# Optimization experiments

Measured on AMD Instinct MI355X. Metric: run time of the kernel, lower is better.

Reference implementation:

```python
import jax, jax.numpy as jnp
import numpy as np

# Static problem sizes (see shape_source)
B, SX, SY = 256, 256, 70          # graphs, encoder nodes/graph, decoder nodes/graph
F, EMB, H = 512, 256, 256          # f_size, emb_size, h_size
VOCAB = 256
E = 4 * B * SY                     # 71680 edges
N_SLT = 4                          # SltEdgeTypes
N_SRT = 8                          # len(SrtEdgeTypes)


def setup_inputs() -> dict:
    key = jax.random.key(0)
    ks = jax.random.split(key, 24)
    s = 0.02
    inp = {
        'x': jax.random.normal(ks[0], (B * SX, F), jnp.float32),
        'x_batch': jnp.repeat(jnp.arange(B, dtype=jnp.int64), SX),
        'tgt_y': jax.random.randint(ks[1], (B * SY,), 0, VOCAB, jnp.int64),
        'tgt_edge_index': jax.random.randint(ks[2], (2, E), 0, B * SY, jnp.int64),
        'tgt_edge_type': jax.random.randint(ks[3], (E,), 0, N_SLT, jnp.int64),
        'tgt_y_batch': jnp.repeat(jnp.arange(B, dtype=jnp.int64), SY),
        'embeds': jax.random.normal(ks[4], (VOCAB, EMB), jnp.float32) * s,
    }
    dims = [(EMB, H), (H, H), (H, EMB)]
    k = 5
    for l, (din, dout) in enumerate(dims, start=1):
        inp[f'W_in{l}'] = jax.random.normal(ks[k + 0], (din, dout), jnp.float32) * s
        inp[f'Wq{l}'] = jax.random.normal(ks[k + 1], (dout, F), jnp.float32) * s
        inp[f'Wv{l}'] = jax.random.normal(ks[k + 2], (F, dout), jnp.float32) * s
        inp[f'Ee{l}'] = jax.random.normal(ks[k + 3], (N_SLT, dout), jnp.float32) * s
        k += 4
    inp['lin_z_w'] = jax.random.normal(ks[k], (EMB, VOCAB), jnp.float32) * s
    inp['lin_z_b'] = jnp.zeros((VOCAB,), jnp.float32)
    inp['lin_g_w'] = jax.random.normal(ks[k + 1], (2 * EMB, N_SRT), jnp.float32) * s
    inp['lin_g_b'] = jnp.zeros((N_SRT,), jnp.float32)
    return inp


def gcn_dec_layer(x_b, y, src, tgt, etype, W_in, Wq, Wv, Ee):
    """Edge-type-conditioned message passing + cross-attention onto encoder x.
    x_b: [B,SX,F]; y: [Ny,din]. Returns ([Ny,dout], alpha [B,SY,SX])."""
    h = y @ W_in                                   # [Ny, dout]
    m = h[src] + Ee[etype]                         # gather + type embedding
    agg = jax.ops.segment_sum(m, tgt, num_segments=y.shape[0])
    q = (h @ Wq).reshape(B, SY, F)                 # query into encoder space
    logits = jnp.einsum('bqf,bkf->bqk', q, x_b) / jnp.sqrt(jnp.float32(F))
    alpha = jax.nn.softmax(logits, axis=-1)        # [B,SY,SX]
    ctx = jnp.einsum('bqk,bkf->bqf', alpha, x_b) @ Wv  # [B,SY,dout]
    out = jax.nn.relu(h + agg + ctx.reshape(h.shape[0], -1))
    return out, alpha


def reference(x, x_batch, tgt_y, tgt_edge_index, tgt_edge_type, tgt_y_batch,
              embeds, W_in1, Wq1, Wv1, Ee1, W_in2, Wq2, Wv2, Ee2,
              W_in3, Wq3, Wv3, Ee3, lin_z_w, lin_z_b, lin_g_w, lin_g_b):
    x_b = x.reshape(B, SX, F)
    src, tgt = tgt_edge_index[0], tgt_edge_index[1]
    y = embeds[tgt_y]                              # [Ny, EMB]
    y, a1 = gcn_dec_layer(x_b, y, src, tgt, tgt_edge_type, W_in1, Wq1, Wv1, Ee1)
    y, a2 = gcn_dec_layer(x_b, y, src, tgt, tgt_edge_type, W_in2, Wq2, Wv2, Ee2)
    y, a3 = gcn_dec_layer(x_b, y, src, tgt, tgt_edge_type, W_in3, Wq3, Wv3, Ee3)
    y_score = y @ lin_z_w + lin_z_b                # [Ny, VOCAB]
    ef = y[tgt_edge_index]                         # [2, E, EMB]
    ef = jnp.transpose(ef, (1, 0, 2)).reshape(E, 2 * EMB)
    y_edge_rel_score = ef @ lin_g_w + lin_g_b      # [E, N_SRT]
    return (y, y_score, y_edge_rel_score, a1, a2, a3)
```

## Files before the change

### kernel.cpp

```cpp
#include <hip/hip_runtime.h>
#include <cstddef>
#include <cstdint>

#define B_    256
#define SX_   256
#define SY_   70
#define F_    512
#define EMB_  256
#define NY_   (B_*SY_)
#define NE_   (4*B_*SY_)

typedef short s16x8 __attribute__((ext_vector_type(8)));
typedef float f32x4 __attribute__((ext_vector_type(4)));
typedef unsigned short us4 __attribute__((ext_vector_type(4)));
typedef unsigned short us8 __attribute__((ext_vector_type(8)));

__device__ __forceinline__ unsigned short f2bf(float f) {
    unsigned u = __builtin_bit_cast(unsigned, f);
    u += 0x7fffu + ((u >> 16) & 1u);
    return (unsigned short)(u >> 16);
}
__device__ __forceinline__ float bf2f(unsigned short b) {
    unsigned u = ((unsigned)b) << 16;
    return __builtin_bit_cast(float, u);
}

template<int EPI, int SWZ>
__global__ __launch_bounds__(256, 2)
void gemm_mfma(const unsigned short* __restrict__ A, int lda, long sAb,
               const unsigned short* __restrict__ Bt, int ldb, long sBb,
               float* __restrict__ Cf, int ldc, long sCfb,
               unsigned short* __restrict__ Cb, int ldcb, long sCbb,
               const float* __restrict__ aux1, long sAux,
               int M, int K, float scale, int nx, int ny)
{
    __shared__ unsigned short As[128 * 64];
    __shared__ unsigned short Bs[128 * 64];
    char* AsB = (char*)As;
    char* BsB = (char*)Bs;
    const int tid = threadIdx.x;
    int bxi, byi, z;
    if (SWZ) {
        const int nwg = gridDim.x;
        const int bid = blockIdx.x;
        const int wg = (bid & 7) * (nwg >> 3) + (bid >> 3);
        bxi = wg % nx;
        byi = (wg / nx) % ny;
        z   = wg / (nx * ny);
    } else {
        bxi = blockIdx.x; byi = blockIdx.y; z = blockIdx.z;
    }
    A  += (size_t)z * sAb;
    Bt += (size_t)z * sBb;
    const char* auxp = (const char*)aux1 + (size_t)z * sAux;
    const int bm = byi * 128, bn = bxi * 128;
    const int lane = tid & 63;
    const int w = tid >> 6, wr = w >> 1, wc = w & 1;
    const int l15 = lane & 15, lq = lane >> 4;

    f32x4 acc[4][4];
    const f32x4 z4 = {0.f, 0.f, 0.f, 0.f};
#pragma unroll
    for (int m = 0; m < 4; ++m)
#pragma unroll
        for (int n = 0; n < 4; ++n) acc[m][n] = z4;

    for (int k0 = 0; k0 < K; k0 += 64) {
#pragma unroll
        for (int i = 0; i < 4; ++i) {
            const int row = i * 32 + (tid >> 3);
            const int k8  = (tid & 7) ^ (row & 7);
            int ra = bm + row; ra = (ra < M) ? ra : (M - 1);
            const unsigned short* g = A + (size_t)ra * lda + k0 + k8 * 8;
            __builtin_amdgcn_global_load_lds(
                (const __attribute__((address_space(1))) unsigned int*)g,
                (__attribute__((address_space(3))) unsigned int*)(AsB + i * 4096 + tid * 16),
                16, 0, 0);
        }
#pragma unroll
        for (int i = 0; i < 4; ++i) {
            const int row = i * 32 + (tid >> 3);
            const int k8  = (tid & 7) ^ (row & 7);
            const unsigned short* g = Bt + (size_t)(bn + row) * ldb + k0 + k8 * 8;
            __builtin_amdgcn_global_load_lds(
                (const __attribute__((address_space(1))) unsigned int*)g,
                (__attribute__((address_space(3))) unsigned int*)(BsB + i * 4096 + tid * 16),
                16, 0, 0);
        }
        __syncthreads();
#pragma unroll
        for (int kk = 0; kk < 2; ++kk) {
            s16x8 af[4], bf[4];
#pragma unroll
            for (int m = 0; m < 4; ++m) {
                const int row = wr * 64 + m * 16 + l15;
                const int slot = (kk * 4 + lq) ^ (row & 7);
                af[m] = *(const s16x8*)(AsB + row * 128 + slot * 16);
            }
#pragma unroll
            for (int n = 0; n < 4; ++n) {
                const int col = wc * 64 + n * 16 + l15;
                const int slot = (kk * 4 + lq) ^ (col & 7);
                bf[n] = *(const s16x8*)(BsB + col * 128 + slot * 16);
            }
#pragma unroll
            for (int m = 0; m < 4; ++m)
#pragma unroll
                for (int n = 0; n < 4; ++n)
                    acc[m][n] = __builtin_amdgcn_mfma_f32_16x16x32_bf16(
                        af[m], bf[n], acc[m][n], 0, 0, 0);
        }
        __syncthreads();
    }

    float* cf = Cf ? Cf + (size_t)z * sCfb : nullptr;
    unsigned short* cb = Cb ? Cb + (size_t)z * sCbb : nullptr;
#pragma unroll
    for (int m = 0; m < 4; ++m) {
#pragma unroll
        for (int n = 0; n < 4; ++n) {
            const int col = bn + wc * 64 + n * 16 + l15;
            f32x4 v = acc[m][n];
#pragma unroll
            for (int r = 0; r < 4; ++r) {
                const int gr = bm + wr * 64 + m * 16 + lq * 4 + r;
                if (gr >= M) continue;
                float o = v[r] * scale;
                if (EPI == 4) o += ((const float*)auxp)[col];
                if (EPI == 7) {
                    if (col < 256) cb[(size_t)gr * ldcb + col] = f2bf(o);
                    else ((unsigned short*)cf)[(size_t)gr * 512 + (col - 256)] = f2bf(o);
                } else {
                    if (cf) cf[(size_t)gr * ldc + col] = o;
                    if (cb) cb[(size_t)gr * ldcb + col] = f2bf(o);
                }
            }
        }
    }
}

template<int LAST>
__global__ __launch_bounds__(512, 1)
void attn_pv(const unsigned short* __restrict__ Q,
             const unsigned short* __restrict__ X,
             const unsigned short* __restrict__ XV,
             long sXVb,
             const unsigned short* __restrict__ aggb,
             const unsigned short* __restrict__ lzT,
             const float* __restrict__ lzb,
             const float* __restrict__ gw,
             float* __restrict__ Y12g,
             float* __restrict__ Aout,
             unsigned short* __restrict__ Yb,
             float* __restrict__ Yf,
             float* __restrict__ Score,
             float scale)
{
    __shared__ unsigned short As[128 * 64];
    __shared__ unsigned short Bs[256 * 64];
    __shared__ unsigned short Al[128 * 256];
    __shared__ float red[4][2][64];
    char* AsB = (char*)As;
    char* BsB = (char*)Bs;
    char* AlB = (char*)Al;
    const int tid = threadIdx.x;
    const int z = blockIdx.x;
    const unsigned short* Qb  = Q + (size_t)z * SY_ * F_;
    const unsigned short* Xb  = X + (size_t)z * SX_ * F_;
    const unsigned short* xvb = XV + (size_t)z * sXVb;
    const int lane = tid & 63;
    const int w = tid >> 6, wr = w >> 2, wc = w & 3;
    const int l15 = lane & 15, lq = lane >> 4;

    f32x4 acc[4][4];
    const f32x4 z4 = {0.f, 0.f, 0.f, 0.f};
#pragma unroll
    for (int m = 0; m < 4; ++m)
#pragma unroll
        for (int n = 0; n < 4; ++n) acc[m][n] = z4;

    for (int k0 = 0; k0 < F_; k0 += 64) {
#pragma unroll
        for (int i = 0; i < 2; ++i) {
            const int row = i * 64 + (tid >> 3);
            const int k8  = (tid & 7) ^ (row & 7);
            const int ra = (row < SY_) ? row : (SY_ - 1);
            const unsigned short* g = Qb + (size_t)ra * F_ + k0 + k8 * 8;
            __builtin_amdgcn_global_load_lds(
                (const __attribute__((address_space(1))) unsigned int*)g,
                (__attribute__((address_space(3))) unsigned int*)(AsB + i * 8192 + tid * 16),
                16, 0, 0);
        }
#pragma unroll
        for (int i = 0; i < 4; ++i) {
            const int row = i * 64 + (tid >> 3);
            const int k8  = (tid & 7) ^ (row & 7);
            const unsigned short* g = Xb + (size_t)row * F_ + k0 + k8 * 8;
            __builtin_amdgcn_global_load_lds(
                (const __attribute__((address_space(1))) unsigned int*)g,
                (__attribute__((address_space(3))) unsigned int*)(BsB + i * 8192 + tid * 16),
                16, 0, 0);
        }
        __syncthreads();
#pragma unroll
        for (int kk = 0; kk < 2; ++kk) {
            s16x8 af[4], bf[4];
#pragma unroll
            for (int m = 0; m < 4; ++m) {
                const int row = wr * 64 + m * 16 + l15;
                const int slot = (kk * 4 + lq) ^ (row & 7);
                af[m] = *(const s16x8*)(AsB + row * 128 + slot * 16);
            }
#pragma unroll
            for (int n = 0; n < 4; ++n) {
                const int col = wc * 64 + n * 16 + l15;
                const int slot = (kk * 4 + lq) ^ (col & 7);
                bf[n] = *(const s16x8*)(BsB + col * 128 + slot * 16);
            }
#pragma unroll
            for (int m = 0; m < 4; ++m)
#pragma unroll
                for (int n = 0; n < 4; ++n)
                    acc[m][n] = __builtin_amdgcn_mfma_f32_16x16x32_bf16(
                        af[m], bf[n], acc[m][n], 0, 0, 0);
        }
        __syncthreads();
    }

#pragma unroll
    for (int m = 0; m < 4; ++m)
#pragma unroll
        for (int n = 0; n < 4; ++n)
#pragma unroll
            for (int r = 0; r < 4; ++r) acc[m][n][r] *= scale;

    float rmax[4][4];
#pragma unroll
    for (int m = 0; m < 4; ++m)
#pragma unroll
        for (int r = 0; r < 4; ++r) {
            float mx = acc[m][0][r];
#pragma unroll
            for (int n = 1; n < 4; ++n) mx = fmaxf(mx, acc[m][n][r]);
            mx = fmaxf(mx, __shfl_xor(mx, 1));
            mx = fmaxf(mx, __shfl_xor(mx, 2));
            mx = fmaxf(mx, __shfl_xor(mx, 4));
            mx = fmaxf(mx, __shfl_xor(mx, 8));
            rmax[m][r] = mx;
        }
    if (l15 == 0) {
#pragma unroll
        for (int m = 0; m < 4; ++m)
#pragma unroll
            for (int r = 0; r < 4; ++r)
                red[wc][wr][m * 16 + lq * 4 + r] = rmax[m][r];
    }
    __syncthreads();
    float rtot[4][4];
#pragma unroll
    for (int m = 0; m < 4; ++m)
#pragma unroll
        for (int r = 0; r < 4; ++r) {
            const int lr = m * 16 + lq * 4 + r;
            rtot[m][r] = fmaxf(fmaxf(red[0][wr][lr], red[1][wr][lr]),
                               fmaxf(red[2][wr][lr], red[3][wr][lr]));
        }
    __syncthreads();
    float rsum[4][4];
#pragma unroll
    for (int m = 0; m < 4; ++m)
#pragma unroll
        for (int r = 0; r < 4; ++r) {
            float s = 0.f;
#pragma unroll
            for (int n = 0; n < 4; ++n) {
                float e = __expf(acc[m][n][r] - rtot[m][r]);
                acc[m][n][r] = e;
                s += e;
            }
            s += __shfl_xor(s, 1);
            s += __shfl_xor(s, 2);
            s += __shfl_xor(s, 4);
            s += __shfl_xor(s, 8);
            rsum[m][r] = s;
        }
    if (l15 == 0) {
#pragma unroll
        for (int m = 0; m < 4; ++m)
#pragma unroll
            for (int r = 0; r < 4; ++r)
                red[wc][wr][m * 16 + lq * 4 + r] = rsum[m][r];
    }
    __syncthreads();
    float* ao = Aout + (size_t)z * SY_ * SX_;
#pragma unroll
    for (int m = 0; m < 4; ++m)
#pragma unroll
        for (int r = 0; r < 4; ++r) {
            const int lr = m * 16 + lq * 4 + r;
            const int row = wr * 64 + lr;
            const float inv = 1.0f / (red[0][wr][lr] + red[1][wr][lr] +
                                      red[2][wr][lr] + red[3][wr][lr]);
#pragma unroll
            for (int n = 0; n < 4; ++n) {
                const int col = wc * 64 + n * 16 + l15;
                const float o = acc[m][n][r] * inv;
                if (row < SY_) ao[(size_t)row * SX_ + col] = o;
                *(unsigned short*)(AlB + row * 512 +
                    (((col >> 3) ^ (row & 7)) << 4) + ((col & 7) << 1)) = f2bf(o);
            }
        }
    __syncthreads();

    f32x4 oac[4][4];
#pragma unroll
    for (int m = 0; m < 4; ++m)
#pragma unroll
        for (int n = 0; n < 4; ++n) oac[m][n] = z4;

    for (int ks = 0; ks < 4; ++ks) {
        const int k0 = ks * 64;
#pragma unroll
        for (int i = 0; i < 4; ++i) {
            const int row = i * 64 + (tid >> 3);
            const int k8  = (tid & 7) ^ (row & 7);
            const unsigned short* g = xvb + (size_t)row * 256 + k0 + k8 * 8;
            __builtin_amdgcn_global_load_lds(
                (const __attribute__((address_space(1))) unsigned int*)g,
                (__attribute__((address_space(3))) unsigned int*)(BsB + i * 8192 + tid * 16),
                16, 0, 0);
        }
        __syncthreads();
#pragma unroll
        for (int kk = 0; kk < 2; ++kk) {
            s16x8 af[4], bf[4];
#pragma unroll
            for (int m = 0; m < 4; ++m) {
                const int row = wr * 64 + m * 16 + l15;
                const int chunk = (k0 >> 3) + kk * 4 + lq;
                af[m] = *(const s16x8*)(AlB + row * 512 + ((chunk ^ (row & 7)) << 4));
            }
#pragma unroll
            for (int n = 0; n < 4; ++n) {
                const int col = wc * 64 + n * 16 + l15;
                const int slot = (kk * 4 + lq) ^ (col & 7);
                bf[n] = *(const s16x8*)(BsB + col * 128 + slot * 16);
            }
#pragma unroll
            for (int m = 0; m < 4; ++m)
#pragma unroll
                for (int n = 0; n < 4; ++n)
                    oac[m][n] = __builtin_amdgcn_mfma_f32_16x16x32_bf16(
                        af[m], bf[n], oac[m][n], 0, 0, 0);
        }
        __syncthreads();
    }

#pragma unroll
    for (int m = 0; m < 4; ++m)
#pragma unroll
        for (int n = 0; n < 4; ++n) {
            const int col = wc * 64 + n * 16 + l15;
            f32x4 v = oac[m][n];
#pragma unroll
            for (int r = 0; r < 4; ++r) {
                const int row = wr * 64 + m * 16 + lq * 4 + r;
                if (row >= SY_) continue;
                const size_t node = (size_t)z * SY_ + row;
                float o = v[r] + bf2f(aggb[node * 256 + col]);
                o = fmaxf(o, 0.f);
                const unsigned short ob = f2bf(o);
                Yb[node * 256 + col] = ob;
                if (Yf) Yf[node * 256 + col] = o;
                if (LAST)
                    *(unsigned short*)(AlB + row * 512 +
                        (((col >> 3) ^ (row & 7)) << 4) + ((col & 7) << 1)) = ob;
            }
        }

    if (LAST) {
        __syncthreads();
#pragma unroll
        for (int m = 0; m < 4; ++m)
#pragma unroll
            for (int n = 0; n < 4; ++n) oac[m][n] = z4;
        for (int ks = 0; ks < 4; ++ks) {
            const int k0 = ks * 64;
#pragma unroll
            for (int i = 0; i < 4; ++i) {
                const int row = i * 64 + (tid >> 3);
                const int k8  = (tid & 7) ^ (row & 7);
                const unsigned short* g = lzT + (size_t)row * 256 + k0 + k8 * 8;
                __builtin_amdgcn_global_load_lds(
                    (const __attribute__((address_space(1))) unsigned int*)g,
                    (__attribute__((address_space(3))) unsigned int*)(BsB + i * 8192 + tid * 16),
                    16, 0, 0);
            }
            __syncthreads();
#pragma unroll
            for (int kk = 0; kk < 2; ++kk) {
                s16x8 af[4], bf[4];
#pragma unroll
                for (int m = 0; m < 4; ++m) {
                    const int row = wr * 64 + m * 16 + l15;
                    const int chunk = (k0 >> 3) + kk * 4 + lq;
                    af[m] = *(const s16x8*)(AlB + row * 512 + ((chunk ^ (row & 7)) << 4));
                }
#pragma unroll
                for (int n = 0; n < 4; ++n) {
                    const int col = wc * 64 + n * 16 + l15;
                    const int slot = (kk * 4 + lq) ^ (col & 7);
                    bf[n] = *(const s16x8*)(BsB + col * 128 + slot * 16);
                }
#pragma unroll
                for (int m = 0; m < 4; ++m)
#pragma unroll
                    for (int n = 0; n < 4; ++n)
                        oac[m][n] = __builtin_amdgcn_mfma_f32_16x16x32_bf16(
                            af[m], bf[n], oac[m][n], 0, 0, 0);
            }
            __syncthreads();
        }
#pragma unroll
        for (int m = 0; m < 4; ++m)
#pragma unroll
            for (int n = 0; n < 4; ++n) {
                const int col = wc * 64 + n * 16 + l15;
                f32x4 v = oac[m][n];
#pragma unroll
                for (int r = 0; r < 4; ++r) {
                    const int row = wr * 64 + m * 16 + lq * 4 + r;
                    if (row >= SY_) continue;
                    Score[((size_t)z * SY_ + row) * 256 + col] = v[r] + lzb[col];
                }
            }

        __syncthreads();
        float* Ws = (float*)BsB;
        for (int i = tid; i < 1024; i += 512)
            ((float4*)Ws)[i] = ((const float4*)gw)[i];
        __syncthreads();
        for (int t = tid; t < 1120; t += 512) {
            const int row = t >> 4, j = t & 15;
            const float* Wcol = Ws + ((j < 8) ? j : (2048 + j - 8));
            float a2 = 0.f;
            for (int c = 0; c < 256; ++c) {
                const float yv = bf2f(*(const unsigned short*)(AlB + row * 512 +
                    (((c >> 3) ^ (row & 7)) << 4) + ((c & 7) << 1)));
                a2 = fmaf(yv, Wcol[c * 8], a2);
            }
            Y12g[((size_t)z * SY_ + row) * 16 + j] = a2;
        }
    }
}

__global__ __launch_bounds__(256)
void conv_x_embed(const float* __restrict__ in, unsigned short* __restrict__ out,
                  int n8, const float* __restrict__ embeds,
                  const int* __restrict__ tgt_y, unsigned short* __restrict__ yb)
{
    if (blockIdx.x < 2048) {
        for (int i = blockIdx.x * 256 + threadIdx.x; i < n8; i += 2048 * 256) {
            float4 a = ((const float4*)in)[i * 2];
            float4 b = ((const float4*)in)[i * 2 + 1];
            us8 o = { f2bf(a.x), f2bf(a.y), f2bf(a.z), f2bf(a.w),
                      f2bf(b.x), f2bf(b.y), f2bf(b.z), f2bf(b.w) };
            ((us8*)out)[i] = o;
        }
    } else {
        const int i = (blockIdx.x - 2048) * 8 + (threadIdx.x >> 5);
        const int c8 = (threadIdx.x & 31) * 8;
        const int v = tgt_y[i];
        const float* p = embeds + (size_t)v * 256 + c8;
        float4 a = *(const float4*)p;
        float4 b = *(const float4*)(p + 4);
        us8 o = { f2bf(a.x), f2bf(a.y), f2bf(a.z), f2bf(a.w),
                  f2bf(b.x), f2bf(b.y), f2bf(b.z), f2bf(b.w) };
        *(us8*)(yb + (size_t)i * 256 + c8) = o;
    }
}

struct WAll {
    const float* src[10];
    unsigned short* dst[10];
    int R[10];
    int C[10];
};

__global__ __launch_bounds__(256)
void conv_wT_all(WAll d)
{
    const int z = blockIdx.z;
    const int R = d.R[z], C = d.C[z];
    const int c0 = blockIdx.x * 64, r0 = blockIdx.y * 64;
    if (c0 >= C || r0 >= R) return;
    const float* in = d.src[z];
    unsigned short* outT = d.dst[z];
    __shared__ unsigned short t[64][65];
    const int r = threadIdx.x >> 4, cq = (threadIdx.x & 15) << 2;
#pragma unroll
    for (int i = 0; i < 4; ++i) {
        const int rr = r + i * 16;
        float4 v = *(const float4*)(in + (size_t)(r0 + rr) * C + c0 + cq);
        t[rr][cq + 0] = f2bf(v.x); t[rr][cq + 1] = f2bf(v.y);
        t[rr][cq + 2] = f2bf(v.z); t[rr][cq + 3] = f2bf(v.w);
    }
    __syncthreads();
    const int c = threadIdx.x >> 2, sq = (threadIdx.x & 3) << 4;
    us8 o0, o1;
#pragma unroll
    for (int i = 0; i < 8; ++i) { o0[i] = t[sq + i][c]; o1[i] = t[sq + 8 + i][c]; }
    *(us8*)(outT + (size_t)(c0 + c) * R + r0 + sq) = o0;
    *(us8*)(outT + (size_t)(c0 + c) * R + r0 + sq + 8) = o1;
}

__global__ __launch_bounds__(256)
void edge_deg(const int* __restrict__ tgt, int* __restrict__ deg)
{
    const int e = blockIdx.x * 256 + threadIdx.x;
    if (e < NE_) atomicAdd(&deg[tgt[e]], 1);
}

__global__ __launch_bounds__(1024)
void scan_off(const int* __restrict__ deg, int* __restrict__ off, int* __restrict__ cursor)
{
    __shared__ int ls[1024];
    const int t = threadIdx.x;
    const int base = t * 18;
    int local[18];
    int s = 0;
#pragma unroll
    for (int i = 0; i < 18; ++i) {
        const int idx = base + i;
        const int v = (idx < NY_) ? deg[idx] : 0;
        local[i] = s; s += v;
    }
    ls[t] = s;
    __syncthreads();
    for (int d = 1; d < 1024; d <<= 1) {
        int v = (t >= d) ? ls[t - d] : 0;
        __syncthreads();
        ls[t] += v;
        __syncthreads();
    }
    const int excl = (t == 0) ? 0 : ls[t - 1];
#pragma unroll
    for (int i = 0; i < 18; ++i) {
        const int idx = base + i;
        if (idx < NY_) {
            const int o = excl + local[i];
            off[idx] = o; cursor[idx] = o;
        }
    }
    if (t == 1023) off[NY_] = ls[1023];
}

__global__ __launch_bounds__(256)
void edge_fill(const int* __restrict__ tgt, int* __restrict__ cursor,
               int* __restrict__ elist)
{
    const int e = blockIdx.x * 256 + threadIdx.x;
    if (e >= NE_) return;
    const int pos = atomicAdd(&cursor[tgt[e]], 1);
    elist[pos] = e;
}

__global__ __launch_bounds__(256)
void node_agg(const unsigned short* __restrict__ hb,
              const float* __restrict__ Ee,
              const int* __restrict__ src, const int* __restrict__ etype,
              const int* __restrict__ off, const int* __restrict__ elist,
              unsigned short* __restrict__ aggb)
{
    const int nid  = blockIdx.x * 4 + (threadIdx.x >> 6);
    const int lane = threadIdx.x & 63;
    const int c = lane * 4;
    const int k0 = off[nid], k1 = off[nid + 1];
    us4 sv = *(const us4*)(hb + (size_t)nid * 256 + c);
    float4 acc;
    acc.x = bf2f(sv[0]); acc.y = bf2f(sv[1]);
    acc.z = bf2f(sv[2]); acc.w = bf2f(sv[3]);
    int cnt0 = 0, cnt1 = 0, cnt2 = 0, cnt3 = 0;
    for (int k = k0; k < k1; ++k) {
        const int e = elist[k];
        const int sfrom = src[e];
        const int ty = etype[e];
        us4 hv = *(const us4*)(hb + (size_t)sfrom * 256 + c);
        acc.x += bf2f(hv[0]); acc.y += bf2f(hv[1]);
        acc.z += bf2f(hv[2]); acc.w += bf2f(hv[3]);
        cnt0 += (ty == 0); cnt1 += (ty == 1); cnt2 += (ty == 2); cnt3 += (ty == 3);
    }
    float4 e0 = *(const float4*)(Ee + c);
    float4 e1 = *(const float4*)(Ee + 256 + c);
    float4 e2 = *(const float4*)(Ee + 512 + c);
    float4 e3 = *(const float4*)(Ee + 768 + c);
    acc.x += cnt0 * e0.x + cnt1 * e1.x + cnt2 * e2.x + cnt3 * e3.x;
    acc.y += cnt0 * e0.y + cnt1 * e1.y + cnt2 * e2.y + cnt3 * e3.y;
    acc.z += cnt0 * e0.z + cnt1 * e1.z + cnt2 * e2.z + cnt3 * e3.z;
    acc.w += cnt0 * e0.w + cnt1 * e1.w + cnt2 * e2.w + cnt3 * e3.w;
    us4 o = { f2bf(acc.x), f2bf(acc.y), f2bf(acc.z), f2bf(acc.w) };
    *(us4*)(aggb + (size_t)nid * 256 + c) = o;
}

__global__ __launch_bounds__(256)
void edge_gather(const float* __restrict__ Y12, const int* __restrict__ src,
                 const int* __restrict__ tgt, const float* __restrict__ bias,
                 float* __restrict__ esc)
{
    const int e = blockIdx.x * 256 + threadIdx.x;
    if (e >= NE_) return;
    const float* a = Y12 + (size_t)src[e] * 16;
    const float* b = Y12 + (size_t)tgt[e] * 16 + 8;
    float4 a0 = ((const float4*)a)[0], a1 = ((const float4*)a)[1];
    float4 b0 = ((const float4*)b)[0], b1 = ((const float4*)b)[1];
    float4 c0 = ((const float4*)bias)[0], c1 = ((const float4*)bias)[1];
    float4 o0, o1;
    o0.x = a0.x + b0.x + c0.x; o0.y = a0.y + b0.y + c0.y;
    o0.z = a0.z + b0.z + c0.z; o0.w = a0.w + b0.w + c0.w;
    o1.x = a1.x + b1.x + c1.x; o1.y = a1.y + b1.y + c1.y;
    o1.z = a1.z + b1.z + c1.z; o1.w = a1.w + b1.w + c1.w;
    ((float4*)(esc + (size_t)e * 8))[0] = o0;
    ((float4*)(esc + (size_t)e * 8))[1] = o1;
}

extern "C" void kernel_launch(void* const* d_in, const int* in_sizes, int n_in,
                              void* d_out, int out_size, void* d_ws, size_t ws_size,
                              hipStream_t stream)
{
    const float* x       = (const float*)d_in[0];
    const int*   tgt_y   = (const int*)d_in[2];
    const int*   eidx    = (const int*)d_in[3];
    const int*   etype   = (const int*)d_in[4];
    const float* embeds  = (const float*)d_in[6];
    const float* W_in[3] = {(const float*)d_in[7],  (const float*)d_in[11], (const float*)d_in[15]};
    const float* Wq[3]   = {(const float*)d_in[8],  (const float*)d_in[12], (const float*)d_in[16]};
    const float* Wv[3]   = {(const float*)d_in[9],  (const float*)d_in[13], (const float*)d_in[17]};
    const float* Ee[3]   = {(const float*)d_in[10], (const float*)d_in[14], (const float*)d_in[18]};
    const float* lin_z_w = (const float*)d_in[19];
    const float* lin_z_b = (const float*)d_in[20];
    const float* lin_g_w = (const float*)d_in[21];
    const float* lin_g_b = (const float*)d_in[22];
    const int* src = eidx;
    const int* tgt = eidx + NE_;

    float* out = (float*)d_out;
    float* y_final = out;
    float* score   = out + 4587520;
    float* esc     = out + 9175040;
    float* aout[3] = {out + 9748480, out + 14336000, out + 18923520};

    char* wsb = (char*)d_ws;
    unsigned short* xb     = (unsigned short*)(wsb + 0);
    unsigned short* xvTall = (unsigned short*)(wsb + 67108864);
    unsigned short* hb     = (unsigned short*)(wsb + 167772160);
    unsigned short* aggb   = (unsigned short*)(wsb + 176947200);
    unsigned short* qb     = (unsigned short*)(wsb + 186122240);
    unsigned short* yb     = (unsigned short*)(wsb + 204472320);
    char* wt = wsb + 213647360;
    unsigned short* wcatT[3], *wqT[3], *wvT[3];
    for (int l = 0; l < 3; ++l) {
        wcatT[l] = (unsigned short*)(wt + l * 393216);
        wqT[l]   = (unsigned short*)(wt + 1179648 + l * 262144);
        wvT[l]   = (unsigned short*)(wt + 1966080 + l * 262144);
    }
    unsigned short* lzT = (unsigned short*)(wt + 2752512);
    char* extra = wsb + 216530944;
    float* Y12    = (float*)extra;
    int*   deg    = (int*)(extra + 1146880);
    int*   off    = (int*)(extra + 1218560);
    int*   cursor = (int*)(extra + 1290244);
    int*   elist  = (int*)(extra + 1361924);

    hipMemsetAsync(deg, 0, NY_ * sizeof(int), stream);
    edge_deg<<<280, 256, 0, stream>>>(tgt, deg);
    scan_off<<<1, 1024, 0, stream>>>(deg, off, cursor);
    edge_fill<<<280, 256, 0, stream>>>(tgt, cursor, elist);

    conv_x_embed<<<4288, 256, 0, stream>>>(x, xb, 4194304, embeds, tgt_y, yb);
    WAll wd;
    for (int l = 0; l < 3; ++l) {
        wd.src[l]     = W_in[l]; wd.dst[l]     = wcatT[l]; wd.R[l]     = 256; wd.C[l]     = 256;
        wd.src[3 + l] = Wq[l];   wd.dst[3 + l] = wqT[l];   wd.R[3 + l] = 256; wd.C[3 + l] = 512;
        wd.src[6 + l] = Wv[l];   wd.dst[6 + l] = wvT[l];   wd.R[6 + l] = 512; wd.C[6 + l] = 256;
    }
    wd.src[9] = lin_z_w; wd.dst[9] = lzT; wd.R[9] = 256; wd.C[9] = 256;
    conv_wT_all<<<dim3(8, 8, 10), 256, 0, stream>>>(wd);

    gemm_mfma<0, 0><<<dim3(2, 4, 3), 256, 0, stream>>>(
        wqT[0], 256, 131072L,  wcatT[0], 256, 196608L,
        nullptr, 0, 0,  wcatT[0] + 65536, 256, 196608L,
        nullptr, 0, 512, 256, 1.f, 0, 0);

    gemm_mfma<0, 1><<<3072, 256, 0, stream>>>(
        wvT[0], 512, 0,  xb, 512, (long)SX_ * F_,
        nullptr, 0, 0,  xvTall, 256, 768L * 256,
        nullptr, 0, 768, 512, 1.f, 2, 6);

    const float qscale = 0.044194173824159216f;
    for (int l = 0; l < 3; ++l) {
        gemm_mfma<7, 0><<<dim3(6, 140, 1), 256, 0, stream>>>(
            yb, 256, 0,  wcatT[l], 256, 0,
            (float*)qb, 512, 0,  hb, 256, 0,
            nullptr, 0, NY_, 256, 1.f, 0, 0);
        node_agg<<<4480, 256, 0, stream>>>(hb, Ee[l], src, etype, off, elist, aggb);
        if (l < 2) {
            attn_pv<0><<<256, 512, 0, stream>>>(
                qb, xb, xvTall + (size_t)l * 65536, 768L * 256,
                aggb, nullptr, nullptr, nullptr, nullptr,
                aout[l], yb, nullptr, nullptr, qscale);
        } else {
            attn_pv<1><<<256, 512, 0, stream>>>(
                qb, xb, xvTall + (size_t)l * 65536, 768L * 256,
                aggb, lzT, lin_z_b, lin_g_w, Y12,
                aout[l], yb, y_final, score, qscale);
        }
    }
    edge_gather<<<280, 256, 0, stream>>>(Y12, src, tgt, lin_g_b, esc);
}
```

Baseline: 437.3 us.

## Double-buffer LDS tiles in attention, PV and score GEMM loops

Adds double buffering to the three K-loops of the fused attention kernel. Global-to-LDS loads for the next tile are issued before the MFMAs on the current tile, so load latency can overlap compute and one barrier per iteration is dropped. The QK loop reuses the idle Al buffer as its second set of buffers, and a new Bs2 buffer serves the PV and score loops. The extra LDS raises per-block footprint, but the kernel already runs one block per CU.

```diff
diff --git a/kernel.cpp b/kernel.cpp
--- a/kernel.cpp
+++ b/kernel.cpp
@@ -158,11 +158,13 @@
 {
     __shared__ unsigned short As[128 * 64];
     __shared__ unsigned short Bs[256 * 64];
+    __shared__ unsigned short Bs2[256 * 64];
     __shared__ unsigned short Al[128 * 256];
     __shared__ float red[4][2][64];
-    char* AsB = (char*)As;
-    char* BsB = (char*)Bs;
-    char* AlB = (char*)Al;
+    char* AsB  = (char*)As;
+    char* BsB  = (char*)Bs;
+    char* Bs2B = (char*)Bs2;
+    char* AlB  = (char*)Al;
     const int tid = threadIdx.x;
     const int z = blockIdx.x;
     const unsigned short* Qb  = Q + (size_t)z * SY_ * F_;
@@ -172,14 +174,12 @@
     const int w = tid >> 6, wr = w >> 2, wc = w & 3;
     const int l15 = lane & 15, lq = lane >> 4;
 
-    f32x4 acc[4][4];
-    const f32x4 z4 = {0.f, 0.f, 0.f, 0.f};
-#pragma unroll
-    for (int m = 0; m < 4; ++m)
-#pragma unroll
-        for (int n = 0; n < 4; ++n) acc[m][n] = z4;
-
-    for (int k0 = 0; k0 < F_; k0 += 64) {
+    char* a_buf[2] = {AsB, AlB};
+    char* b_buf[2] = {BsB, AlB + 16384};
+
+    auto stage1 = [&](int k0, int buf) {
+        char* ab = a_buf[buf];
+        char* bb = b_buf[buf];
 #pragma unroll
         for (int i = 0; i < 2; ++i) {
             const int row = i * 64 + (tid >> 3);
@@ -188,7 +188,7 @@
             const unsigned short* g = Qb + (size_t)ra * F_ + k0 + k8 * 8;
             __builtin_amdgcn_global_load_lds(
                 (const __attribute__((address_space(1))) unsigned int*)g,
-                (__attribute__((address_space(3))) unsigned int*)(AsB + i * 8192 + tid * 16),
+                (__attribute__((address_space(3))) unsigned int*)(ab + i * 8192 + tid * 16),
                 16, 0, 0);
         }
 #pragma unroll
@@ -198,10 +198,25 @@
             const unsigned short* g = Xb + (size_t)row * F_ + k0 + k8 * 8;
             __builtin_amdgcn_global_load_lds(
                 (const __attribute__((address_space(1))) unsigned int*)g,
-                (__attribute__((address_space(3))) unsigned int*)(BsB + i * 8192 + tid * 16),
+                (__attribute__((address_space(3))) unsigned int*)(bb + i * 8192 + tid * 16),
                 16, 0, 0);
         }
-        __syncthreads();
+    };
+
+    f32x4 acc[4][4];
+    const f32x4 z4 = {0.f, 0.f, 0.f, 0.f};
+#pragma unroll
+    for (int m = 0; m < 4; ++m)
+#pragma unroll
+        for (int n = 0; n < 4; ++n) acc[m][n] = z4;
+
+    stage1(0, 0);
+    __syncthreads();
+    int cur = 0;
+    for (int t = 0; t < 8; ++t) {
+        if (t < 7) stage1((t + 1) * 64, cur ^ 1);
+        char* ab = a_buf[cur];
+        char* bb = b_buf[cur];
 #pragma unroll
         for (int kk = 0; kk < 2; ++kk) {
             s16x8 af[4], bf[4];
@@ -209,13 +224,13 @@
             for (int m = 0; m < 4; ++m) {
                 const int row = wr * 64 + m * 16 + l15;
                 const int slot = (kk * 4 + lq) ^ (row & 7);
-                af[m] = *(const s16x8*)(AsB + row * 128 + slot * 16);
+                af[m] = *(const s16x8*)(ab + row * 128 + slot * 16);
             }
 #pragma unroll
             for (int n = 0; n < 4; ++n) {
                 const int col = wc * 64 + n * 16 + l15;
                 const int slot = (kk * 4 + lq) ^ (col & 7);
-                bf[n] = *(const s16x8*)(BsB + col * 128 + slot * 16);
+                bf[n] = *(const s16x8*)(bb + col * 128 + slot * 16);
             }
 #pragma unroll
             for (int m = 0; m < 4; ++m)
@@ -225,6 +240,7 @@
                         af[m], bf[n], acc[m][n], 0, 0, 0);
         }
         __syncthreads();
+        cur ^= 1;
     }
 
 #pragma unroll
@@ -312,25 +328,34 @@
         }
     __syncthreads();
 
-    f32x4 oac[4][4];
-#pragma unroll
-    for (int m = 0; m < 4; ++m)
-#pragma unroll
-        for (int n = 0; n < 4; ++n) oac[m][n] = z4;
-
-    for (int ks = 0; ks < 4; ++ks) {
-        const int k0 = ks * 64;
+    char* v_buf[2] = {BsB, Bs2B};
+    auto stage2 = [&](int k0, int buf, const unsigned short* srcm) {
+        char* bb = v_buf[buf];
 #pragma unroll
         for (int i = 0; i < 4; ++i) {
             const int row = i * 64 + (tid >> 3);
             const int k8  = (tid & 7) ^ (row & 7);
-            const unsigned short* g = xvb + (size_t)row * 256 + k0 + k8 * 8;
+            const unsigned short* g = srcm + (size_t)row * 256 + k0 + k8 * 8;
             __builtin_amdgcn_global_load_lds(
                 (const __attribute__((address_space(1))) unsigned int*)g,
-                (__attribute__((address_space(3))) unsigned int*)(BsB + i * 8192 + tid * 16),
+                (__attribute__((address_space(3))) unsigned int*)(bb + i * 8192 + tid * 16),
                 16, 0, 0);
         }
-        __syncthreads();
+    };
+
+    f32x4 oac[4][4];
+#pragma unroll
+    for (int m = 0; m < 4; ++m)
+#pragma unroll
+        for (int n = 0; n < 4; ++n) oac[m][n] = z4;
+
+    stage2(0, 0, xvb);
+    __syncthreads();
+    cur = 0;
+    for (int ks = 0; ks < 4; ++ks) {
+        if (ks < 3) stage2((ks + 1) * 64, cur ^ 1, xvb);
+        char* bb = v_buf[cur];
+        const int k0 = ks * 64;
 #pragma unroll
         for (int kk = 0; kk < 2; ++kk) {
             s16x8 af[4], bf[4];
@@ -344,7 +369,7 @@
             for (int n = 0; n < 4; ++n) {
                 const int col = wc * 64 + n * 16 + l15;
                 const int slot = (kk * 4 + lq) ^ (col & 7);
-                bf[n] = *(const s16x8*)(BsB + col * 128 + slot * 16);
+                bf[n] = *(const s16x8*)(bb + col * 128 + slot * 16);
             }
 #pragma unroll
             for (int m = 0; m < 4; ++m)
@@ -354,6 +379,7 @@
                         af[m], bf[n], oac[m][n], 0, 0, 0);
         }
         __syncthreads();
+        cur ^= 1;
     }
 
 #pragma unroll
@@ -384,19 +410,13 @@
         for (int m = 0; m < 4; ++m)
 #pragma unroll
             for (int n = 0; n < 4; ++n) oac[m][n] = z4;
+        stage2(0, 0, lzT);
+        __syncthreads();
+        cur = 0;
         for (int ks = 0; ks < 4; ++ks) {
+            if (ks < 3) stage2((ks + 1) * 64, cur ^ 1, lzT);
+            char* bb = v_buf[cur];
             const int k0 = ks * 64;
-#pragma unroll
-            for (int i = 0; i < 4; ++i) {
-                const int row = i * 64 + (tid >> 3);
-                const int k8  = (tid & 7) ^ (row & 7);
-                const unsigned short* g = lzT + (size_t)row * 256 + k0 + k8 * 8;
-                __builtin_amdgcn_global_load_lds(
-                    (const __attribute__((address_space(1))) unsigned int*)g,
-                    (__attribute__((address_space(3))) unsigned int*)(BsB + i * 8192 + tid * 16),
-                    16, 0, 0);
-            }
-            __syncthreads();
 #pragma unroll
             for (int kk = 0; kk < 2; ++kk) {
                 s16x8 af[4], bf[4];
@@ -410,7 +430,7 @@
                 for (int n = 0; n < 4; ++n) {
                     const int col = wc * 64 + n * 16 + l15;
                     const int slot = (kk * 4 + lq) ^ (col & 7);
-                    bf[n] = *(const s16x8*)(BsB + col * 128 + slot * 16);
+                    bf[n] = *(const s16x8*)(bb + col * 128 + slot * 16);
                 }
 #pragma unroll
                 for (int m = 0; m < 4; ++m)
@@ -420,6 +440,7 @@
                             af[m], bf[n], oac[m][n], 0, 0, 0);
             }
             __syncthreads();
+            cur ^= 1;
         }
 #pragma unroll
         for (int m = 0; m < 4; ++m)
```

New measurement: 435.6 us. No clear change (-0.4%).
